# Kernel tuning notes

Measured on AMD Instinct MI355X. Metric: run time of the kernel, lower is better.

The kernel has to match this reference:

```python
import jax, jax.numpy as jnp
import numpy as np

B, C, N = 8, 256, 2048
H = max(1, C // 8)  # hidden = in_channels // 8 = 32


def setup_inputs() -> dict:
    key = jax.random.key(0)
    ks = jax.random.split(key, 7)
    s = 0.05
    return {
        "x": jax.random.normal(ks[0], (B, C, N), dtype=jnp.float32),
        "wq": jax.random.normal(ks[1], (H, C), dtype=jnp.float32) * s,
        "bq": jax.random.normal(ks[2], (H,), dtype=jnp.float32) * s,
        "wk": jax.random.normal(ks[3], (H, C), dtype=jnp.float32) * s,
        "bk": jax.random.normal(ks[4], (H,), dtype=jnp.float32) * s,
        "wv": jax.random.normal(ks[5], (C, C), dtype=jnp.float32) * s,
        "bv": jax.random.normal(ks[6], (C,), dtype=jnp.float32) * s,
    }


def reference(x, wq, bq, wk, bk, wv, bv):
    # 1x1 Conv1d == per-position linear: weight [out, in]
    q = jnp.einsum('bcn,hc->bnh', x, wq) + bq                  # [B, N, H] (already permuted)
    k = jnp.einsum('bcn,hc->bhn', x, wk) + bk[None, :, None]   # [B, H, N]
    v = jnp.einsum('bcn,dc->bdn', x, wv) + bv[None, :, None]   # [B, C, N]
    energy = jnp.einsum('bnh,bhm->bnm', q, k)                  # [B, N, N] (no scaling, as in source)
    weights = jax.nn.softmax(energy, axis=-1)                  # softmax over last dim
    # out = bmm(value, weights^T): out[b,c,i] = sum_j v[b,c,j] * weights[b,i,j]
    out = jnp.einsum('bcj,bij->bci', v, weights)               # [B, C, N]
    return out + x
```

## Files before the change

### kernel.cpp

```cpp
#include <hip/hip_runtime.h>
#include <hip/hip_bf16.h>
#include <cstdint>
#include <cstddef>

#define B_ 8
#define C_ 256
#define N_ 2048
#define H_ 32
#define VP_ 2064
#define NT_ (N_ / 64)

typedef __bf16 bf8 __attribute__((ext_vector_type(8)));
typedef __bf16 bf4 __attribute__((ext_vector_type(4)));
typedef float f4 __attribute__((ext_vector_type(4)));

__device__ inline void gload_lds16(const void* g, void* l) {
  __builtin_amdgcn_global_load_lds(
      (const __attribute__((address_space(1))) unsigned int*)g,
      (__attribute__((address_space(3))) unsigned int*)l, 16, 0, 0);
}

__global__ __launch_bounds__(256) void pack_kernel(
    const float* __restrict__ wq, const float* __restrict__ wk,
    const float* __restrict__ wv, const float* __restrict__ bq,
    const float* __restrict__ bk, const float* __restrict__ bv,
    __hip_bfloat16* __restrict__ wpk, float* __restrict__ bpk) {
  const float L2E = 1.44269504088896f;
  int r = blockIdx.x, c = threadIdx.x;
  float v;
  if (r < 256)      v = wv[r * 256 + c];
  else if (r < 288) v = wq[(r - 256) * 256 + c] * L2E;
  else              v = wk[(r - 288) * 256 + c];
  wpk[r * 256 + c] = __float2bfloat16(v);
  if (c == 0) bpk[r] = (r < 256) ? bv[r] : (r < 288 ? bq[r - 256] * L2E : bk[r - 288]);
}

__global__ __launch_bounds__(256) void proj_kernel(
    const float* __restrict__ x, const __hip_bfloat16* __restrict__ wpk,
    const float* __restrict__ bpk, __hip_bfloat16* __restrict__ vbf,
    __hip_bfloat16* __restrict__ qkb) {
  __shared__ __attribute__((aligned(16))) __hip_bfloat16 As[3][320 * 32];
  __shared__ __attribute__((aligned(16))) float xS[4][32 * 32];
  int tid = threadIdx.x, wv = tid >> 6, lane = tid & 63;
  int b = blockIdx.y;
  int n0 = blockIdx.x * 32;
  int fcol = lane & 15, hi4 = lane >> 4;
  int grow = lane >> 2, gc = (lane & 3) * 8;
  int xrow = wv * 8 + (lane >> 3), xcq = (lane & 7) * 4;
  const float* xb = x + (size_t)b * C_ * N_;

#define STAGE_W(T)                                                            \
  _Pragma("unroll")                                                           \
  for (int g = 0; g < 5; ++g)                                                 \
    gload_lds16(wpk + (size_t)(wv * 80 + g * 16 + grow) * 256 + (T) * 32 + gc,\
                &As[(T) % 3][(wv * 80 + g * 16) * 32]);
#define STAGE_X(T)                                                            \
  gload_lds16(xb + (size_t)((T) * 32 + xrow) * N_ + n0 + xcq,                 \
              &xS[(T) % 4][wv * 8 * 32]);

  STAGE_X(0)
  STAGE_W(0)
  STAGE_X(1)
  STAGE_W(1)
  STAGE_X(2)

  f4 acc[5][2] = {};
#pragma unroll
  for (int t = 0; t < 8; ++t) {
    if (t < 6)      asm volatile("s_waitcnt vmcnt(7)" ::: "memory");
    else if (t == 6) asm volatile("s_waitcnt vmcnt(6)" ::: "memory");
    else            asm volatile("s_waitcnt vmcnt(0)" ::: "memory");
    __builtin_amdgcn_s_barrier();
    __builtin_amdgcn_sched_barrier(0);
    if (t + 2 <= 7) { STAGE_W(t + 2) }
    if (t + 3 <= 7) { STAGE_X(t + 3) }
    const float* xt = &xS[t % 4][0];
    bf8 bfr[2];
#pragma unroll
    for (int j = 0; j < 2; ++j)
#pragma unroll
      for (int e = 0; e < 8; ++e)
        bfr[j][e] = (__bf16)xt[(hi4 * 8 + e) * 32 + j * 16 + fcol];
#pragma unroll
    for (int s = 0; s < 5; ++s) {
      bf8 af = *(const bf8*)&As[t % 3][(wv * 80 + s * 16 + fcol) * 32 + hi4 * 8];
      acc[s][0] = __builtin_amdgcn_mfma_f32_16x16x32_bf16(af, bfr[0], acc[s][0], 0, 0, 0);
      acc[s][1] = __builtin_amdgcn_mfma_f32_16x16x32_bf16(af, bfr[1], acc[s][1], 0, 0, 0);
    }
  }
#undef STAGE_W
#undef STAGE_X
  int rq = hi4 * 4;
#pragma unroll
  for (int s = 0; s < 5; ++s)
#pragma unroll
    for (int r = 0; r < 4; ++r) {
      int m = wv * 80 + s * 16 + rq + r;
      float bias = bpk[m];
#pragma unroll
      for (int j = 0; j < 2; ++j) {
        int n = n0 + j * 16 + fcol;
        float val = acc[s][j][r] + bias;
        if (m < 256)
          vbf[((size_t)b * C_ + m) * VP_ + n] = __float2bfloat16(val);
        else
          qkb[((size_t)b * N_ + n) * 64 + (m - 256)] = __float2bfloat16(val);
      }
    }
}

#define MFMA16(A, B, C) __builtin_amdgcn_mfma_f32_16x16x32_bf16(A, B, C, 0, 0, 0)

#define ATTN_BODY(T, BUF, KC, KN, VA, VB, VC, VD)                              \
  {                                                                            \
    bf8 pf00 = *(const bf8*)&pS[BUF][ 0 + li][ 0 + lg8];                       \
    bf8 pf10 = *(const bf8*)&pS[BUF][16 + li][ 0 + lg8];                       \
    bf8 pf01 = *(const bf8*)&pS[BUF][ 0 + li][32 + lg8];                       \
    bf8 pf11 = *(const bf8*)&pS[BUF][16 + li][32 + lg8];                       \
    f4 s0 = {}, s1 = {};                                                       \
    if ((T) + 1 < NT_) {                                                       \
      s0 = MFMA16(KC, qf0, s0);                                                \
      s1 = MFMA16(KC, qf1, s1);                                                \
    }                                                                          \
    {                                                                          \
      int tn_ = (T) + 2 < NT_ ? (T) + 2 : NT_ - 1;                             \
      KN = *(const bf8*)(kp + (size_t)tn_ * 64 * 64);                          \
    }                                                                          \
    __builtin_amdgcn_s_setprio(1);                                             \
    acc[0][0] = MFMA16(VA, pf00, acc[0][0]);                                   \
    acc[0][1] = MFMA16(VA, pf10, acc[0][1]);                                   \
    acc[1][0] = MFMA16(VC, pf00, acc[1][0]);                                   \
    acc[1][1] = MFMA16(VC, pf10, acc[1][1]);                                   \
    acc[0][0] = MFMA16(VB, pf01, acc[0][0]);                                   \
    acc[0][1] = MFMA16(VB, pf11, acc[0][1]);                                   \
    acc[1][0] = MFMA16(VD, pf01, acc[1][0]);                                   \
    acc[1][1] = MFMA16(VD, pf11, acc[1][1]);                                   \
    __builtin_amdgcn_s_setprio(0);                                             \
    {                                                                          \
      int tn_ = (T) + 2 < NT_ ? (T) + 2 : NT_ - 1;                             \
      const __hip_bfloat16* vpn_ = vR + tn_ * 64;                              \
      VA = *(const bf8*)vpn_;                                                  \
      VB = *(const bf8*)(vpn_ + 32);                                           \
      VC = *(const bf8*)(vpn_ + 16 * VP_);                                     \
      VD = *(const bf8*)(vpn_ + 16 * VP_ + 32);                                \
    }                                                                          \
    if ((T) + 1 < NT_) {                                                       \
      _Pragma("unroll")                                                        \
      for (int m = 0; m < 4; ++m) {                                            \
        s0[m] = __builtin_amdgcn_exp2f(s0[m]);                                 \
        s1[m] = __builtin_amdgcn_exp2f(s1[m]);                                 \
      }                                                                        \
      lp0 += s0[0] + s0[1] + s0[2] + s0[3];                                    \
      lp1 += s1[0] + s1[1] + s1[2] + s1[3];                                    \
      bf4 t0, t1;                                                              \
      _Pragma("unroll")                                                        \
      for (int m = 0; m < 4; ++m) { t0[m] = (__bf16)s0[m]; t1[m] = (__bf16)s1[m]; } \
      *(bf4*)&pS[(BUF) ^ 1][ 0 + li][wv * 16 + lg4] = t0;                      \
      *(bf4*)&pS[(BUF) ^ 1][16 + li][wv * 16 + lg4] = t1;                      \
      asm volatile("s_waitcnt lgkmcnt(0)" ::: "memory");                       \
      __builtin_amdgcn_sched_barrier(0);                                       \
      __builtin_amdgcn_s_barrier();                                            \
      __builtin_amdgcn_sched_barrier(0);                                       \
    }                                                                          \
  }

__global__ __launch_bounds__(256, 4) void fused_attn(
    const __hip_bfloat16* __restrict__ qk,
    const __hip_bfloat16* __restrict__ vbf,
    const float* __restrict__ x, float* __restrict__ out) {
  __shared__ __attribute__((aligned(16))) __hip_bfloat16 pS[2][32][72];
  __shared__ float lSp[4][32];
  int tid = threadIdx.x;
  int wv = tid >> 6, lane = tid & 63;
  int li = lane & 15, lg = lane >> 4;
  int lg8 = lg * 8, lg4 = lg * 4;
  int blk = blockIdx.x;
  int b = blk & 7;
  int rest = blk >> 3;
  int c0 = (rest & 1) * 128;
  int i0 = (rest >> 1) * 32;

  const __hip_bfloat16* qkB = qk + (size_t)b * N_ * 64;
  bf8 qf0 = *(const bf8*)&qkB[(size_t)(i0 +  0 + li) * 64 + lg8];
  bf8 qf1 = *(const bf8*)&qkB[(size_t)(i0 + 16 + li) * 64 + lg8];
  const __hip_bfloat16* kp = qkB + (size_t)(wv * 16 + li) * 64 + 32 + lg8;
  const __hip_bfloat16* vR =
      vbf + ((size_t)b * C_ + c0 + wv * 32 + li) * VP_ + lg8;

  bf8 k00 = *(const bf8*)kp;
  bf8 kO = *(const bf8*)(kp + 64 * 64);
  bf8 kE;
  bf8 vEA = *(const bf8*)vR;
  bf8 vEB = *(const bf8*)(vR + 32);
  bf8 vEC = *(const bf8*)(vR + 16 * VP_);
  bf8 vED = *(const bf8*)(vR + 16 * VP_ + 32);
  bf8 vOA = *(const bf8*)(vR + 64);
  bf8 vOB = *(const bf8*)(vR + 64 + 32);
  bf8 vOC = *(const bf8*)(vR + 16 * VP_ + 64);
  bf8 vOD = *(const bf8*)(vR + 16 * VP_ + 64 + 32);

  f4 acc[2][2] = {};
  float lp0 = 0.f, lp1 = 0.f;

  {
    f4 s0 = {}, s1 = {};
    s0 = MFMA16(k00, qf0, s0);
    s1 = MFMA16(k00, qf1, s1);
#pragma unroll
    for (int m = 0; m < 4; ++m) {
      s0[m] = __builtin_amdgcn_exp2f(s0[m]);
      s1[m] = __builtin_amdgcn_exp2f(s1[m]);
    }
    lp0 += s0[0] + s0[1] + s0[2] + s0[3];
    lp1 += s1[0] + s1[1] + s1[2] + s1[3];
    bf4 t0, t1;
#pragma unroll
    for (int m = 0; m < 4; ++m) { t0[m] = (__bf16)s0[m]; t1[m] = (__bf16)s1[m]; }
    *(bf4*)&pS[0][ 0 + li][wv * 16 + lg4] = t0;
    *(bf4*)&pS[0][16 + li][wv * 16 + lg4] = t1;
    asm volatile("s_waitcnt lgkmcnt(0)" ::: "memory");
    __builtin_amdgcn_sched_barrier(0);
    __builtin_amdgcn_s_barrier();
    __builtin_amdgcn_sched_barrier(0);
  }

  for (int tt = 0; tt < NT_; tt += 2) {
    ATTN_BODY(tt,     0, kO, kE, vEA, vEB, vEC, vED)
    ATTN_BODY(tt + 1, 1, kE, kO, vOA, vOB, vOC, vOD)
  }
#undef ATTN_BODY

  lp0 += __shfl_xor(lp0, 16); lp0 += __shfl_xor(lp0, 32);
  lp1 += __shfl_xor(lp1, 16); lp1 += __shfl_xor(lp1, 32);
  if (lane < 16) { lSp[wv][lane] = lp0; lSp[wv][16 + lane] = lp1; }
  __syncthreads();
  float linv0 = 1.0f / (lSp[0][li] + lSp[1][li] + lSp[2][li] + lSp[3][li]);
  float linv1 = 1.0f / (lSp[0][16 + li] + lSp[1][16 + li] +
                        lSp[2][16 + li] + lSp[3][16 + li]);

  const float* xr = x + (size_t)b * C_ * N_;
  float* op = out + (size_t)b * C_ * N_;
#pragma unroll
  for (int cs = 0; cs < 2; ++cs)
#pragma unroll
    for (int m = 0; m < 4; ++m) {
      int c = c0 + wv * 32 + cs * 16 + lg4 + m;
      size_t base = (size_t)c * N_ + i0;
      op[base +  0 + li] = acc[cs][0][m] * linv0 + xr[base +  0 + li];
      op[base + 16 + li] = acc[cs][1][m] * linv1 + xr[base + 16 + li];
    }
}

extern "C" void kernel_launch(void* const* d_in, const int* in_sizes, int n_in,
                              void* d_out, int out_size, void* d_ws, size_t ws_size,
                              hipStream_t stream) {
  const float* x  = (const float*)d_in[0];
  const float* wq = (const float*)d_in[1];
  const float* bq = (const float*)d_in[2];
  const float* wk = (const float*)d_in[3];
  const float* bk = (const float*)d_in[4];
  const float* wv = (const float*)d_in[5];
  const float* bv = (const float*)d_in[6];
  float* out = (float*)d_out;

  char* ws = (char*)d_ws;
  __hip_bfloat16* qkb = (__hip_bfloat16*)ws;
  __hip_bfloat16* vbf = (__hip_bfloat16*)(ws + (2u << 20));
  __hip_bfloat16* wpk = (__hip_bfloat16*)(ws + 10551296u);
  float*          bpk = (float*)(ws + 10551296u + 163840u);

  pack_kernel<<<dim3(320), 256, 0, stream>>>(wq, wk, wv, bq, bk, bv, wpk, bpk);
  proj_kernel<<<dim3(N_ / 32, B_), 256, 0, stream>>>(x, wpk, bpk, vbf, qkb);
  fused_attn<<<dim3(1024), 256, 0, stream>>>(qkb, vbf, x, out);
}
```

Baseline: 147.2 us.

## Widen attention blocks to 64 queries and all 256 channels with 8 waves

Each fused_attn block now handles 64 query rows and the full 256 channels using 512 threads (8 waves) instead of 32 rows by 128 channels with 4 waves. The QK^T scores for the 64x64 tile are split across waves by row pair and column group and shared through a larger LDS buffer, so each score is computed once for all channels rather than recomputed per channel half. Each wave keeps twice as many output accumulators. The intent is to remove redundant score/exp work and K reloads; the cost is fewer blocks (256 on a large GPU), higher register pressure, and a heavier block-wide barrier per tile.

```diff
diff --git a/kernel.cpp b/kernel.cpp
--- a/kernel.cpp
+++ b/kernel.cpp
@@ -115,8 +115,12 @@
   {                                                                            \
     bf8 pf00 = *(const bf8*)&pS[BUF][ 0 + li][ 0 + lg8];                       \
     bf8 pf10 = *(const bf8*)&pS[BUF][16 + li][ 0 + lg8];                       \
+    bf8 pf20 = *(const bf8*)&pS[BUF][32 + li][ 0 + lg8];                       \
+    bf8 pf30 = *(const bf8*)&pS[BUF][48 + li][ 0 + lg8];                       \
     bf8 pf01 = *(const bf8*)&pS[BUF][ 0 + li][32 + lg8];                       \
     bf8 pf11 = *(const bf8*)&pS[BUF][16 + li][32 + lg8];                       \
+    bf8 pf21 = *(const bf8*)&pS[BUF][32 + li][32 + lg8];                       \
+    bf8 pf31 = *(const bf8*)&pS[BUF][48 + li][32 + lg8];                       \
     f4 s0 = {}, s1 = {};                                                       \
     if ((T) + 1 < NT_) {                                                       \
       s0 = MFMA16(KC, qf0, s0);                                                \
@@ -129,12 +133,20 @@
     __builtin_amdgcn_s_setprio(1);                                             \
     acc[0][0] = MFMA16(VA, pf00, acc[0][0]);                                   \
     acc[0][1] = MFMA16(VA, pf10, acc[0][1]);                                   \
+    acc[0][2] = MFMA16(VA, pf20, acc[0][2]);                                   \
+    acc[0][3] = MFMA16(VA, pf30, acc[0][3]);                                   \
     acc[1][0] = MFMA16(VC, pf00, acc[1][0]);                                   \
     acc[1][1] = MFMA16(VC, pf10, acc[1][1]);                                   \
+    acc[1][2] = MFMA16(VC, pf20, acc[1][2]);                                   \
+    acc[1][3] = MFMA16(VC, pf30, acc[1][3]);                                   \
     acc[0][0] = MFMA16(VB, pf01, acc[0][0]);                                   \
     acc[0][1] = MFMA16(VB, pf11, acc[0][1]);                                   \
+    acc[0][2] = MFMA16(VB, pf21, acc[0][2]);                                   \
+    acc[0][3] = MFMA16(VB, pf31, acc[0][3]);                                   \
     acc[1][0] = MFMA16(VD, pf01, acc[1][0]);                                   \
     acc[1][1] = MFMA16(VD, pf11, acc[1][1]);                                   \
+    acc[1][2] = MFMA16(VD, pf21, acc[1][2]);                                   \
+    acc[1][3] = MFMA16(VD, pf31, acc[1][3]);                                   \
     __builtin_amdgcn_s_setprio(0);                                             \
     {                                                                          \
       int tn_ = (T) + 2 < NT_ ? (T) + 2 : NT_ - 1;                             \
@@ -155,8 +167,8 @@
       bf4 t0, t1;                                                              \
       _Pragma("unroll")                                                        \
       for (int m = 0; m < 4; ++m) { t0[m] = (__bf16)s0[m]; t1[m] = (__bf16)s1[m]; } \
-      *(bf4*)&pS[(BUF) ^ 1][ 0 + li][wv * 16 + lg4] = t0;                      \
-      *(bf4*)&pS[(BUF) ^ 1][16 + li][wv * 16 + lg4] = t1;                      \
+      *(bf4*)&pS[(BUF) ^ 1][is0 * 16 + li][js * 16 + lg4] = t0;                \
+      *(bf4*)&pS[(BUF) ^ 1][is0 * 16 + 16 + li][js * 16 + lg4] = t1;           \
       asm volatile("s_waitcnt lgkmcnt(0)" ::: "memory");                       \
       __builtin_amdgcn_sched_barrier(0);                                       \
       __builtin_amdgcn_s_barrier();                                            \
@@ -164,28 +176,28 @@
     }                                                                          \
   }
 
-__global__ __launch_bounds__(256, 4) void fused_attn(
+__global__ __launch_bounds__(512, 2) void fused_attn(
     const __hip_bfloat16* __restrict__ qk,
     const __hip_bfloat16* __restrict__ vbf,
     const float* __restrict__ x, float* __restrict__ out) {
-  __shared__ __attribute__((aligned(16))) __hip_bfloat16 pS[2][32][72];
-  __shared__ float lSp[4][32];
+  __shared__ __attribute__((aligned(16))) __hip_bfloat16 pS[2][64][88];
+  __shared__ float lSp[4][4][16];
   int tid = threadIdx.x;
   int wv = tid >> 6, lane = tid & 63;
   int li = lane & 15, lg = lane >> 4;
   int lg8 = lg * 8, lg4 = lg * 4;
+  int is0 = (wv >> 2) * 2;
+  int js = wv & 3;
   int blk = blockIdx.x;
   int b = blk & 7;
-  int rest = blk >> 3;
-  int c0 = (rest & 1) * 128;
-  int i0 = (rest >> 1) * 32;
+  int i0 = (blk >> 3) * 64;
 
   const __hip_bfloat16* qkB = qk + (size_t)b * N_ * 64;
-  bf8 qf0 = *(const bf8*)&qkB[(size_t)(i0 +  0 + li) * 64 + lg8];
-  bf8 qf1 = *(const bf8*)&qkB[(size_t)(i0 + 16 + li) * 64 + lg8];
-  const __hip_bfloat16* kp = qkB + (size_t)(wv * 16 + li) * 64 + 32 + lg8;
+  bf8 qf0 = *(const bf8*)&qkB[(size_t)(i0 + is0 * 16 + li) * 64 + lg8];
+  bf8 qf1 = *(const bf8*)&qkB[(size_t)(i0 + is0 * 16 + 16 + li) * 64 + lg8];
+  const __hip_bfloat16* kp = qkB + (size_t)(js * 16 + li) * 64 + 32 + lg8;
   const __hip_bfloat16* vR =
-      vbf + ((size_t)b * C_ + c0 + wv * 32 + li) * VP_ + lg8;
+      vbf + ((size_t)b * C_ + wv * 32 + li) * VP_ + lg8;
 
   bf8 k00 = *(const bf8*)kp;
   bf8 kO = *(const bf8*)(kp + 64 * 64);
@@ -199,7 +211,7 @@
   bf8 vOC = *(const bf8*)(vR + 16 * VP_ + 64);
   bf8 vOD = *(const bf8*)(vR + 16 * VP_ + 64 + 32);
 
-  f4 acc[2][2] = {};
+  f4 acc[2][4] = {};
   float lp0 = 0.f, lp1 = 0.f;
 
   {
@@ -216,8 +228,8 @@
     bf4 t0, t1;
 #pragma unroll
     for (int m = 0; m < 4; ++m) { t0[m] = (__bf16)s0[m]; t1[m] = (__bf16)s1[m]; }
-    *(bf4*)&pS[0][ 0 + li][wv * 16 + lg4] = t0;
-    *(bf4*)&pS[0][16 + li][wv * 16 + lg4] = t1;
+    *(bf4*)&pS[0][is0 * 16 + li][js * 16 + lg4] = t0;
+    *(bf4*)&pS[0][is0 * 16 + 16 + li][js * 16 + lg4] = t1;
     asm volatile("s_waitcnt lgkmcnt(0)" ::: "memory");
     __builtin_amdgcn_sched_barrier(0);
     __builtin_amdgcn_s_barrier();
@@ -232,11 +244,16 @@
 
   lp0 += __shfl_xor(lp0, 16); lp0 += __shfl_xor(lp0, 32);
   lp1 += __shfl_xor(lp1, 16); lp1 += __shfl_xor(lp1, 32);
-  if (lane < 16) { lSp[wv][lane] = lp0; lSp[wv][16 + lane] = lp1; }
+  if (lane < 16) {
+    lSp[js][is0][lane] = lp0;
+    lSp[js][is0 + 1][lane] = lp1;
+  }
   __syncthreads();
-  float linv0 = 1.0f / (lSp[0][li] + lSp[1][li] + lSp[2][li] + lSp[3][li]);
-  float linv1 = 1.0f / (lSp[0][16 + li] + lSp[1][16 + li] +
-                        lSp[2][16 + li] + lSp[3][16 + li]);
+  float linv[4];
+#pragma unroll
+  for (int is = 0; is < 4; ++is)
+    linv[is] = 1.0f / (lSp[0][is][li] + lSp[1][is][li] +
+                       lSp[2][is][li] + lSp[3][is][li]);
 
   const float* xr = x + (size_t)b * C_ * N_;
   float* op = out + (size_t)b * C_ * N_;
@@ -244,10 +261,12 @@
   for (int cs = 0; cs < 2; ++cs)
 #pragma unroll
     for (int m = 0; m < 4; ++m) {
-      int c = c0 + wv * 32 + cs * 16 + lg4 + m;
+      int c = wv * 32 + cs * 16 + lg4 + m;
       size_t base = (size_t)c * N_ + i0;
-      op[base +  0 + li] = acc[cs][0][m] * linv0 + xr[base +  0 + li];
-      op[base + 16 + li] = acc[cs][1][m] * linv1 + xr[base + 16 + li];
+      op[base +  0 + li] = acc[cs][0][m] * linv[0] + xr[base +  0 + li];
+      op[base + 16 + li] = acc[cs][1][m] * linv[1] + xr[base + 16 + li];
+      op[base + 32 + li] = acc[cs][2][m] * linv[2] + xr[base + 32 + li];
+      op[base + 48 + li] = acc[cs][3][m] * linv[3] + xr[base + 48 + li];
     }
 }
 
@@ -271,5 +290,5 @@
 
   pack_kernel<<<dim3(320), 256, 0, stream>>>(wq, wk, wv, bq, bk, bv, wpk, bpk);
   proj_kernel<<<dim3(N_ / 32, B_), 256, 0, stream>>>(x, wpk, bpk, vbf, qkb);
-  fused_attn<<<dim3(1024), 256, 0, stream>>>(qkb, vbf, x, out);
-}
+  fused_attn<<<dim3(256), 512, 0, stream>>>(qkb, vbf, x, out);
+}
```

New measurement: 132.9 us. 9.7% less time.
